# Performance work log

Hardware: AMD Instinct MI355X
Metric: run time of the kernel (lower is better)

Reference implementation:

```python
import math
import jax, jax.numpy as jnp
import numpy as np

B, S, D_MODEL, H = 2, 2048, 1024, 16
HD = D_MODEL // H  # head_dim = 64


def setup_inputs() -> dict:
    key = jax.random.key(0)
    ks = jax.random.split(key, 5)
    scale = 1.0 / math.sqrt(D_MODEL)
    return {
        "x": jax.random.normal(ks[0], (B, S, D_MODEL), dtype=jnp.float32),
        "attention_mask": jnp.ones((B, S), dtype=jnp.int32),
        "causal": 1,
        "Wq": jax.random.normal(ks[1], (D_MODEL, D_MODEL), dtype=jnp.float32) * scale,
        "Wk": jax.random.normal(ks[2], (D_MODEL, D_MODEL), dtype=jnp.float32) * scale,
        "Wv": jax.random.normal(ks[3], (D_MODEL, D_MODEL), dtype=jnp.float32) * scale,
        "Wo": jax.random.normal(ks[4], (D_MODEL, D_MODEL), dtype=jnp.float32) * scale,
    }


def reference(x, attention_mask, causal, Wq, Wk, Wv, Wo):
    b, s, d = x.shape
    # QKV projections, split heads -> (b, h, s, hd)
    q = (x @ Wq).reshape(b, s, H, HD).transpose(0, 2, 1, 3)
    k = (x @ Wk).reshape(b, s, H, HD).transpose(0, 2, 1, 3)
    v = (x @ Wv).reshape(b, s, H, HD).transpose(0, 2, 1, 3)

    score = jnp.einsum("bhqd,bhkd->bhqk", q, k) / math.sqrt(HD)

    neg_inf = jnp.float32(-jnp.inf)
    if causal:
        causal_mask = jnp.tril(jnp.ones((s, s), dtype=bool))  # (s, s)
        score = jnp.where(causal_mask[None, None, :, :], score, neg_inf)
    key_mask = attention_mask.astype(bool)[:, None, None, :]  # (b,1,1,s)
    score = jnp.where(key_mask, score, neg_inf)

    attn = jax.nn.softmax(score, axis=-1)  # numerically stable (max-subtracted)
    out = jnp.einsum("bhqk,bhkd->bhqd", attn, v)  # (b,h,s,hd)
    out = out.transpose(0, 2, 1, 3).reshape(b, s, d)
    return out @ Wo
```

## Files before the change

kernel.cpp:

```cpp
#include <hip/hip_runtime.h>
#include <hip/hip_bf16.h>

#define B_  2
#define S_  2048
#define D_  1024
#define H_  16
#define HD_ 64
#define BS_ (B_*S_)

typedef __attribute__((ext_vector_type(8))) short bf16x8;
typedef __attribute__((ext_vector_type(4))) float f32x4;
typedef __attribute__((ext_vector_type(4))) float float4v;
typedef __attribute__((ext_vector_type(4))) unsigned short ushort4v;
typedef __attribute__((ext_vector_type(2))) unsigned int uint2v;

__device__ __forceinline__ unsigned short f2bf(float f) {
  union { float f; unsigned int u; } v; v.f = f;
  unsigned int u = v.u;
  return (unsigned short)((u + 0x7fffu + ((u >> 16) & 1u)) >> 16);
}
__device__ __forceinline__ float bf2f(unsigned short u) {
  union { unsigned int i; float f; } v; v.i = ((unsigned int)u) << 16; return v.f;
}
__device__ __forceinline__ unsigned int cvtpk(float lo, float hi) {
  unsigned int r;
  asm("v_cvt_pk_bf16_f32 %0, %1, %2" : "=v"(r) : "v"(lo), "v"(hi));
  return r;
}

__device__ __forceinline__ void gload16(const void* g, void* l) {
  __builtin_amdgcn_global_load_lds((const __attribute__((address_space(1))) void*)g,
                                   (__attribute__((address_space(3))) void*)l, 16, 0, 0);
}

__device__ __forceinline__ f32x4 mfma16(bf16x8 a, bf16x8 b, f32x4 c) {
  return __builtin_amdgcn_mfma_f32_16x16x32_bf16(a, b, c, 0, 0, 0);
}

__global__ __launch_bounds__(256) void k_prep(const float* __restrict__ x, unsigned short* __restrict__ xb,
                                              const float* __restrict__ w0, const float* __restrict__ w1,
                                              const float* __restrict__ w2, const float* __restrict__ w3,
                                              unsigned short* __restrict__ o0, unsigned short* __restrict__ o1,
                                              unsigned short* __restrict__ o2, unsigned short* __restrict__ o3) {
  const int bid = blockIdx.x;
  if (bid < 2048) {
    int i = bid * 256 + threadIdx.x;
    float4v a = ((const float4v*)x)[2*i];
    float4v b = ((const float4v*)x)[2*i + 1];
    union { bf16x8 v; unsigned short u[8]; } o;
#pragma unroll
    for (int j = 0; j < 4; ++j) { o.u[j] = f2bf(a[j]); o.u[4+j] = f2bf(b[j]); }
    ((bf16x8*)xb)[i] = o.v;
    return;
  }
  const int wid = bid - 2048;
  const int xx = wid & 15, yy = (wid >> 4) & 15, zz = wid >> 8;
  const float* w = zz == 0 ? w0 : zz == 1 ? w1 : zz == 2 ? w2 : w3;
  unsigned short* o = zz == 0 ? o0 : zz == 1 ? o1 : zz == 2 ? o2 : o3;
  __shared__ unsigned short til[64][68];
  const int n0 = xx * 64, k0 = yy * 64;
  const int t = threadIdx.x, r = t >> 4, c4 = t & 15;
#pragma unroll
  for (int i = 0; i < 4; ++i) {
    float4v v = *(const float4v*)(w + (size_t)(k0 + i*16 + r) * D_ + n0 + c4*4);
#pragma unroll
    for (int j = 0; j < 4; ++j) til[i*16 + r][c4*4 + j] = f2bf(v[j]);
  }
  __syncthreads();
#pragma unroll
  for (int i = 0; i < 4; ++i) {
    ushort4v u;
#pragma unroll
    for (int j = 0; j < 4; ++j) u[j] = til[c4*4 + j][i*16 + r];
    *(ushort4v*)(o + (size_t)(n0 + i*16 + r) * D_ + k0 + c4*4) = u;
  }
}

template <int MODE, typename OutT>
__device__ __forceinline__ void gemm_body(const unsigned short* __restrict__ A,
                                          const unsigned short* __restrict__ Bt,
                                          OutT* __restrict__ C,
                                          int M, int N, int K, int mblk, int nblk) {
  __shared__ unsigned short As[128 * 64];
  __shared__ unsigned short Bs[128 * 64];
  const int tid = threadIdx.x;
  const int w = tid >> 6, lane = tid & 63;
  const int lg = lane >> 4, li = lane & 15;
  const int m0 = mblk * 128, n0 = nblk * 128;
  const int wr = (w >> 1) * 64, wc = (w & 1) * 64;
  f32x4 acc[4][4] = {};
  for (int kt = 0; kt < K; kt += 64) {
#pragma unroll
    for (int i = 0; i < 4; ++i) {
      int c = (i*4 + w) * 64 + lane;
      int r = c >> 3, kc = c & 7;
      int off = ((kc ^ (r & 7)) << 3);
      gload16(A  + (size_t)(m0 + r) * K + kt + off, (char*)As + (i*4 + w) * 1024);
      gload16(Bt + (size_t)(n0 + r) * K + kt + off, (char*)Bs + (i*4 + w) * 1024);
    }
    __syncthreads();
#pragma unroll
    for (int ks = 0; ks < 2; ++ks) {
      bf16x8 af[4], bfr[4];
#pragma unroll
      for (int m = 0; m < 4; ++m) {
        int rr = wr + m*16 + li;
        int ch = (ks*4 + lg) ^ (rr & 7);
        af[m] = *(const bf16x8*)((const char*)As + rr*128 + ch*16);
      }
#pragma unroll
      for (int n = 0; n < 4; ++n) {
        int rr = wc + n*16 + li;
        int ch = (ks*4 + lg) ^ (rr & 7);
        bfr[n] = *(const bf16x8*)((const char*)Bs + rr*128 + ch*16);
      }
#pragma unroll
      for (int m = 0; m < 4; ++m)
#pragma unroll
        for (int n = 0; n < 4; ++n)
          acc[m][n] = mfma16(af[m], bfr[n], acc[m][n]);
    }
    __syncthreads();
  }
#pragma unroll
  for (int m = 0; m < 4; ++m)
#pragma unroll
    for (int n = 0; n < 4; ++n) {
      if (MODE == 2) {
        int gr = m0 + wr + m*16 + lg*4;
        int gc = n0 + wc + n*16 + li;
        int bb = gr >> 11, ss = gr & 2047, hh = gc >> 6, dd = gc & 63;
        unsigned short* p = (unsigned short*)C + ((size_t)((bb*H_ + hh)*HD_ + dd)) * S_ + ss;
        uint2v o2;
        o2[0] = cvtpk(acc[m][n][0], acc[m][n][1]);
        o2[1] = cvtpk(acc[m][n][2], acc[m][n][3]);
        *(uint2v*)p = o2;
      } else {
#pragma unroll
        for (int j = 0; j < 4; ++j) {
          int row = m0 + wr + m*16 + lg*4 + j;
          int col = n0 + wc + n*16 + li;
          if (MODE == 1) ((float*)C)[(size_t)row * N + col] = acc[m][n][j];
          else ((unsigned short*)C)[(size_t)row * N + col] = f2bf(acc[m][n][j]);
        }
      }
    }
}

__global__ __launch_bounds__(256, 2) void k_qkv(const unsigned short* __restrict__ xb,
    const unsigned short* __restrict__ wqt, const unsigned short* __restrict__ wkt,
    const unsigned short* __restrict__ wvt,
    unsigned short* __restrict__ Qb, unsigned short* __restrict__ Kb, unsigned short* __restrict__ Vtb) {
  const int z = blockIdx.z;
  if (z == 2) {
    gemm_body<2, unsigned short>(xb, wvt, Vtb, BS_, D_, D_, blockIdx.x, blockIdx.y);
  } else {
    gemm_body<0, unsigned short>(xb, z ? wkt : wqt, z ? Kb : Qb, BS_, D_, D_, blockIdx.x, blockIdx.y);
  }
}

__global__ __launch_bounds__(256, 2) void k_out(const unsigned short* __restrict__ AO,
                                                const unsigned short* __restrict__ wot,
                                                float* __restrict__ out) {
  gemm_body<1, float>(AO, wot, out, BS_, D_, D_, blockIdx.x, blockIdx.y);
}

__global__ __launch_bounds__(256, 4) void k_attn(const unsigned short* __restrict__ Q,
                                                 const unsigned short* __restrict__ K,
                                                 const unsigned short* __restrict__ Vt,
                                                 unsigned short* __restrict__ AO) {
  __shared__ unsigned short Ks[2 * 64 * 64];
  __shared__ unsigned short Vs[2 * 64 * 64];
  __shared__ unsigned short Ps[4 * 16 * 64];
  const int bh = blockIdx.x;
  const int y = blockIdx.y;
  const int qb = (y < 8) ? 31 - y : (y < 16) ? y - 8 : (y < 24) ? 39 - y : y - 16;
  const int b = bh >> 4, h = bh & 15;
  const int tid = threadIdx.x, w = tid >> 6, lane = tid & 63;
  const int lg = lane >> 4, li = lane & 15;
  unsigned short* Psw = Ps + w * 1024;
  const float SC2 = 0.18033688f;

  const unsigned short* qptr = Q + (size_t)(b*S_ + qb*64 + w*16 + li) * D_ + h*HD_;
  union { bf16x8 v; unsigned short u[8]; } q0u, q1u;
  q0u.v = *(const bf16x8*)(qptr + lg*8);
  q1u.v = *(const bf16x8*)(qptr + 32 + lg*8);
#pragma unroll
  for (int j = 0; j < 8; ++j) {
    q0u.u[j] = f2bf(bf2f(q0u.u[j]) * SC2);
    q1u.u[j] = f2bf(bf2f(q1u.u[j]) * SC2);
  }
  const bf16x8 qf0 = q0u.v, qf1 = q1u.v;

  int paddr[8];
#pragma unroll
  for (int kj = 0; kj < 4; ++kj)
#pragma unroll
    for (int hh = 0; hh < 2; ++hh)
      paddr[kj*2 + hh] = li*128 + (((2*kj + (lg >> 1)) ^ (li & 7)) << 4) + (lg & 1)*8 + 4*hh;
  int pboff[2];
#pragma unroll
  for (int ks = 0; ks < 2; ++ks)
    pboff[ks] = li*128 + (((ks*4 + lg) ^ (li & 7)) << 4);

  int kofs[2], vofs[2], lofs[2];
#pragma unroll
  for (int i = 0; i < 2; ++i) {
    int c = (i*4 + w) * 64 + lane;
    int r = c >> 3, kc = c & 7;
    int off = ((kc ^ (r & 7)) << 3);
    kofs[i] = r * D_ + off;
    vofs[i] = r * S_ + off;
    lofs[i] = (i*4 + w) * 1024;
  }
  const unsigned short* kg = K  + (size_t)(b*S_) * D_ + h*HD_;
  const unsigned short* vg = Vt + (size_t)bh * HD_ * S_;

  f32x4 oacc[4] = {};
  float mrow = -1e30f, lrow = 0.f;

  auto stage = [&](int bsel, const unsigned short* kp, const unsigned short* vp) {
    char* KsB = (char*)Ks + bsel * 8192;
    char* VsB = (char*)Vs + bsel * 8192;
#pragma unroll
    for (int i = 0; i < 2; ++i) {
      gload16(kp + kofs[i], KsB + lofs[i]);
      gload16(vp + vofs[i], VsB + lofs[i]);
    }
  };

  stage(0, kg, vg);
  __syncthreads();

  for (int kt = 0; kt <= qb; ++kt) {
    const int cur = kt & 1;
    if (kt < qb) {
      kg += 64 * D_; vg += 64;
      stage(cur ^ 1, kg, vg);
    }
    const char* KsB = (const char*)Ks + cur * 8192;
    const char* VsB = (const char*)Vs + cur * 8192;

    f32x4 sc[4];
    __builtin_amdgcn_s_setprio(1);
#pragma unroll
    for (int kj = 0; kj < 4; ++kj) {
      f32x4 t = {};
      t = mfma16(*(const bf16x8*)(KsB + kj*2048 + pboff[0]), qf0, t);
      t = mfma16(*(const bf16x8*)(KsB + kj*2048 + pboff[1]), qf1, t);
      sc[kj] = t;
    }
    __builtin_amdgcn_s_setprio(0);

    if (kt == qb) {
      const int qloc = w*16 + li;
#pragma unroll
      for (int kj = 0; kj < 4; ++kj)
#pragma unroll
        for (int j = 0; j < 4; ++j)
          if (kj*16 + lg*4 + j > qloc) sc[kj][j] = -1e30f;
    }

    float a0 = fmaxf(fmaxf(sc[0][0], sc[0][1]), sc[0][2]);
    float a1 = fmaxf(fmaxf(sc[0][3], sc[1][0]), sc[1][1]);
    float a2 = fmaxf(fmaxf(sc[1][2], sc[1][3]), sc[2][0]);
    float a3 = fmaxf(fmaxf(sc[2][1], sc[2][2]), sc[2][3]);
    float a4 = fmaxf(fmaxf(sc[3][0], sc[3][1]), sc[3][2]);
    float mx = fmaxf(fmaxf(fmaxf(a0, a1), fmaxf(a2, a3)), fmaxf(a4, sc[3][3]));
    mx = fmaxf(mx, __int_as_float(__builtin_amdgcn_ds_swizzle(__float_as_int(mx), 0x401F)));
    mx = fmaxf(mx, __shfl_xor(mx, 32, 64));
    if (__any(mx > mrow + 8.f)) {
      const float mnew = fmaxf(mrow, mx);
      const float alpha = exp2f(mrow - mnew);
#pragma unroll
      for (int n = 0; n < 4; ++n)
#pragma unroll
        for (int j = 0; j < 4; ++j) oacc[n][j] *= alpha;
      lrow *= alpha;
      mrow = mnew;
    }
    float rs = 0.f;
    f32x4 pv[4];
#pragma unroll
    for (int kj = 0; kj < 4; ++kj)
#pragma unroll
      for (int j = 0; j < 4; ++j) {
        float p = exp2f(sc[kj][j] - mrow);
        rs += p;
        pv[kj][j] = p;
      }
    lrow += rs;

#pragma unroll
    for (int kj = 0; kj < 4; ++kj) {
      *(unsigned int*)((char*)Psw + paddr[kj*2 + 0]) = cvtpk(pv[kj][0], pv[kj][1]);
      *(unsigned int*)((char*)Psw + paddr[kj*2 + 1]) = cvtpk(pv[kj][2], pv[kj][3]);
    }

    const bf16x8 pf0 = *(const bf16x8*)((const char*)Psw + pboff[0]);
    const bf16x8 pf1 = *(const bf16x8*)((const char*)Psw + pboff[1]);
    __builtin_amdgcn_s_setprio(1);
#pragma unroll
    for (int n = 0; n < 4; ++n) {
      oacc[n] = mfma16(*(const bf16x8*)(VsB + n*2048 + pboff[0]), pf0, oacc[n]);
      oacc[n] = mfma16(*(const bf16x8*)(VsB + n*2048 + pboff[1]), pf1, oacc[n]);
    }
    __builtin_amdgcn_s_setprio(0);
    __syncthreads();
  }

  lrow += __int_as_float(__builtin_amdgcn_ds_swizzle(__float_as_int(lrow), 0x401F));
  lrow += __shfl_xor(lrow, 32, 64);
  const float inv = 1.0f / lrow;
  unsigned short* aorow = AO + (size_t)(b*S_ + qb*64 + w*16 + li) * D_ + h*HD_;
#pragma unroll
  for (int n = 0; n < 4; ++n) {
    uint2v o2;
    o2[0] = cvtpk(oacc[n][0] * inv, oacc[n][1] * inv);
    o2[1] = cvtpk(oacc[n][2] * inv, oacc[n][3] * inv);
    *(uint2v*)(aorow + n*16 + lg*4) = o2;
  }
}

extern "C" void kernel_launch(void* const* d_in, const int* in_sizes, int n_in,
                              void* d_out, int out_size, void* d_ws, size_t ws_size,
                              hipStream_t stream) {
  const float* x  = (const float*)d_in[0];
  const float* Wq = (const float*)d_in[3];
  const float* Wk = (const float*)d_in[4];
  const float* Wv = (const float*)d_in[5];
  const float* Wo = (const float*)d_in[6];
  float* out = (float*)d_out;

  unsigned short* ws  = (unsigned short*)d_ws;
  unsigned short* xb  = ws;
  unsigned short* wqt = xb  + (size_t)BS_ * D_;
  unsigned short* wkt = wqt + (size_t)D_ * D_;
  unsigned short* wvt = wkt + (size_t)D_ * D_;
  unsigned short* wot = wvt + (size_t)D_ * D_;
  unsigned short* Qb  = wot + (size_t)D_ * D_;
  unsigned short* Kb  = Qb  + (size_t)BS_ * D_;
  unsigned short* Vtb = Kb  + (size_t)BS_ * D_;
  unsigned short* AO  = Vtb + (size_t)BS_ * D_;

  k_prep<<<3072, 256, 0, stream>>>(x, xb, Wq, Wk, Wv, Wo, wqt, wkt, wvt, wot);
  k_qkv<<<dim3(32, 8, 3), 256, 0, stream>>>(xb, wqt, wkt, wvt, Qb, Kb, Vtb);
  k_attn<<<dim3(32, 32), 256, 0, stream>>>(Qb, Kb, Vtb, AO);
  k_out<<<dim3(32, 8), 256, 0, stream>>>(AO, wot, out);
}
```

Measured before the change: 112.4 us.

## Split attention into 32-query two-wave blocks and use permlane swap reductions

The attention kernel now gives each block 32 query rows handled by two waves instead of 64 rows by four waves, doubling the grid to 64 query tiles. Tiles are launched longest-first by causal length. The aim is finer-grained work for better load balance and occupancy across CUs. The cost is that K/V tiles are staged into LDS twice as often per query. Row max and sum reductions now use gfx950 permlane16/32 swap instructions instead of ds_swizzle plus shfl_xor, which avoids LDS-path cross-lane traffic.

```diff
diff --git a/kernel.cpp b/kernel.cpp
--- a/kernel.cpp
+++ b/kernel.cpp
@@ -26,6 +26,39 @@
   unsigned int r;
   asm("v_cvt_pk_bf16_f32 %0, %1, %2" : "=v"(r) : "v"(lo), "v"(hi));
   return r;
+}
+
+__device__ __forceinline__ void plswap16(float& a, float& b) {
+#if __has_builtin(__builtin_amdgcn_permlane16_swap)
+  uint2v r = __builtin_amdgcn_permlane16_swap(__float_as_uint(a), __float_as_uint(b), false, false);
+  a = __uint_as_float(r[0]); b = __uint_as_float(r[1]);
+#else
+  asm volatile("v_permlane16_swap_b32 %0, %1" : "+v"(a), "+v"(b));
+#endif
+}
+__device__ __forceinline__ void plswap32(float& a, float& b) {
+#if __has_builtin(__builtin_amdgcn_permlane32_swap)
+  uint2v r = __builtin_amdgcn_permlane32_swap(__float_as_uint(a), __float_as_uint(b), false, false);
+  a = __uint_as_float(r[0]); b = __uint_as_float(r[1]);
+#else
+  asm volatile("v_permlane32_swap_b32 %0, %1" : "+v"(a), "+v"(b));
+#endif
+}
+__device__ __forceinline__ float wave_max_lg(float x) {
+  float t;
+  asm volatile("v_mov_b32 %0, %1" : "=v"(t) : "v"(x));
+  plswap16(x, t); x = fmaxf(x, t);
+  asm volatile("v_mov_b32 %0, %1" : "=v"(t) : "v"(x));
+  plswap32(x, t); x = fmaxf(x, t);
+  return x;
+}
+__device__ __forceinline__ float wave_sum_lg(float x) {
+  float t;
+  asm volatile("v_mov_b32 %0, %1" : "=v"(t) : "v"(x));
+  plswap16(x, t); x += t;
+  asm volatile("v_mov_b32 %0, %1" : "=v"(t) : "v"(x));
+  plswap32(x, t); x += t;
+  return x;
 }
 
 __device__ __forceinline__ void gload16(const void* g, void* l) {
@@ -165,23 +198,24 @@
   gemm_body<1, float>(AO, wot, out, BS_, D_, D_, blockIdx.x, blockIdx.y);
 }
 
-__global__ __launch_bounds__(256, 4) void k_attn(const unsigned short* __restrict__ Q,
+__global__ __launch_bounds__(128, 2) void k_attn(const unsigned short* __restrict__ Q,
                                                  const unsigned short* __restrict__ K,
                                                  const unsigned short* __restrict__ Vt,
                                                  unsigned short* __restrict__ AO) {
   __shared__ unsigned short Ks[2 * 64 * 64];
   __shared__ unsigned short Vs[2 * 64 * 64];
-  __shared__ unsigned short Ps[4 * 16 * 64];
+  __shared__ unsigned short Ps[2 * 16 * 64];
   const int bh = blockIdx.x;
-  const int y = blockIdx.y;
-  const int qb = (y < 8) ? 31 - y : (y < 16) ? y - 8 : (y < 24) ? 39 - y : y - 16;
+  const int qb = 63 - blockIdx.y;
+  const int nkt = (qb >> 1) + 1;
   const int b = bh >> 4, h = bh & 15;
   const int tid = threadIdx.x, w = tid >> 6, lane = tid & 63;
   const int lg = lane >> 4, li = lane & 15;
   unsigned short* Psw = Ps + w * 1024;
   const float SC2 = 0.18033688f;
 
-  const unsigned short* qptr = Q + (size_t)(b*S_ + qb*64 + w*16 + li) * D_ + h*HD_;
+  const int qglob = qb*32 + w*16 + li;
+  const unsigned short* qptr = Q + (size_t)(b*S_ + qglob) * D_ + h*HD_;
   union { bf16x8 v; unsigned short u[8]; } q0u, q1u;
   q0u.v = *(const bf16x8*)(qptr + lg*8);
   q1u.v = *(const bf16x8*)(qptr + 32 + lg*8);
@@ -203,15 +237,14 @@
   for (int ks = 0; ks < 2; ++ks)
     pboff[ks] = li*128 + (((ks*4 + lg) ^ (li & 7)) << 4);
 
-  int kofs[2], vofs[2], lofs[2];
-#pragma unroll
-  for (int i = 0; i < 2; ++i) {
-    int c = (i*4 + w) * 64 + lane;
+  int kofs[4], vofs[4];
+#pragma unroll
+  for (int i = 0; i < 4; ++i) {
+    int c = i*128 + tid;
     int r = c >> 3, kc = c & 7;
     int off = ((kc ^ (r & 7)) << 3);
     kofs[i] = r * D_ + off;
     vofs[i] = r * S_ + off;
-    lofs[i] = (i*4 + w) * 1024;
   }
   const unsigned short* kg = K  + (size_t)(b*S_) * D_ + h*HD_;
   const unsigned short* vg = Vt + (size_t)bh * HD_ * S_;
@@ -223,18 +256,18 @@
     char* KsB = (char*)Ks + bsel * 8192;
     char* VsB = (char*)Vs + bsel * 8192;
 #pragma unroll
-    for (int i = 0; i < 2; ++i) {
-      gload16(kp + kofs[i], KsB + lofs[i]);
-      gload16(vp + vofs[i], VsB + lofs[i]);
+    for (int i = 0; i < 4; ++i) {
+      gload16(kp + kofs[i], KsB + (i*2 + w) * 1024);
+      gload16(vp + vofs[i], VsB + (i*2 + w) * 1024);
     }
   };
 
   stage(0, kg, vg);
   __syncthreads();
 
-  for (int kt = 0; kt <= qb; ++kt) {
+  for (int kt = 0; kt < nkt; ++kt) {
     const int cur = kt & 1;
-    if (kt < qb) {
+    if (kt + 1 < nkt) {
       kg += 64 * D_; vg += 64;
       stage(cur ^ 1, kg, vg);
     }
@@ -252,23 +285,21 @@
     }
     __builtin_amdgcn_s_setprio(0);
 
-    if (kt == qb) {
-      const int qloc = w*16 + li;
+    if (kt == nkt - 1) {
+      const int qrel = qglob - kt*64;
 #pragma unroll
       for (int kj = 0; kj < 4; ++kj)
 #pragma unroll
         for (int j = 0; j < 4; ++j)
-          if (kj*16 + lg*4 + j > qloc) sc[kj][j] = -1e30f;
-    }
-
-    float a0 = fmaxf(fmaxf(sc[0][0], sc[0][1]), sc[0][2]);
-    float a1 = fmaxf(fmaxf(sc[0][3], sc[1][0]), sc[1][1]);
-    float a2 = fmaxf(fmaxf(sc[1][2], sc[1][3]), sc[2][0]);
-    float a3 = fmaxf(fmaxf(sc[2][1], sc[2][2]), sc[2][3]);
-    float a4 = fmaxf(fmaxf(sc[3][0], sc[3][1]), sc[3][2]);
-    float mx = fmaxf(fmaxf(fmaxf(a0, a1), fmaxf(a2, a3)), fmaxf(a4, sc[3][3]));
-    mx = fmaxf(mx, __int_as_float(__builtin_amdgcn_ds_swizzle(__float_as_int(mx), 0x401F)));
-    mx = fmaxf(mx, __shfl_xor(mx, 32, 64));
+          if (kj*16 + lg*4 + j > qrel) sc[kj][j] = -1e30f;
+    }
+
+    float mx = sc[0][0];
+#pragma unroll
+    for (int kj = 0; kj < 4; ++kj)
+#pragma unroll
+      for (int j = 0; j < 4; ++j) mx = fmaxf(mx, sc[kj][j]);
+    mx = wave_max_lg(mx);
     if (__any(mx > mrow + 8.f)) {
       const float mnew = fmaxf(mrow, mx);
       const float alpha = exp2f(mrow - mnew);
@@ -279,8 +310,8 @@
       lrow *= alpha;
       mrow = mnew;
     }
+    f32x4 pv[4];
     float rs = 0.f;
-    f32x4 pv[4];
 #pragma unroll
     for (int kj = 0; kj < 4; ++kj)
 #pragma unroll
@@ -302,17 +333,18 @@
     __builtin_amdgcn_s_setprio(1);
 #pragma unroll
     for (int n = 0; n < 4; ++n) {
-      oacc[n] = mfma16(*(const bf16x8*)(VsB + n*2048 + pboff[0]), pf0, oacc[n]);
-      oacc[n] = mfma16(*(const bf16x8*)(VsB + n*2048 + pboff[1]), pf1, oacc[n]);
+      int vr = n*16 + li;
+      int ch0 = lg ^ (vr & 7), ch1 = (4 + lg) ^ (vr & 7);
+      oacc[n] = mfma16(*(const bf16x8*)(VsB + vr*128 + ch0*16), pf0, oacc[n]);
+      oacc[n] = mfma16(*(const bf16x8*)(VsB + vr*128 + ch1*16), pf1, oacc[n]);
     }
     __builtin_amdgcn_s_setprio(0);
     __syncthreads();
   }
 
-  lrow += __int_as_float(__builtin_amdgcn_ds_swizzle(__float_as_int(lrow), 0x401F));
-  lrow += __shfl_xor(lrow, 32, 64);
+  lrow = wave_sum_lg(lrow);
   const float inv = 1.0f / lrow;
-  unsigned short* aorow = AO + (size_t)(b*S_ + qb*64 + w*16 + li) * D_ + h*HD_;
+  unsigned short* aorow = AO + (size_t)(b*S_ + qglob) * D_ + h*HD_;
 #pragma unroll
   for (int n = 0; n < 4; ++n) {
     uint2v o2;
@@ -345,6 +377,6 @@
 
   k_prep<<<3072, 256, 0, stream>>>(x, xb, Wq, Wk, Wv, Wo, wqt, wkt, wvt, wot);
   k_qkv<<<dim3(32, 8, 3), 256, 0, stream>>>(xb, wqt, wkt, wvt, Qb, Kb, Vtb);
-  k_attn<<<dim3(32, 32), 256, 0, stream>>>(Qb, Kb, Vtb, AO);
+  k_attn<<<dim3(32, 64), 128, 0, stream>>>(Qb, Kb, Vtb, AO);
   k_out<<<dim3(32, 8), 256, 0, stream>>>(AO, wot, out);
 }
```

After: 117.9 us. 1.05x slower.
